# Performance work log

Hardware: AMD Instinct MI355X
Metric: run time of the kernel (lower is better)

Reference implementation:

```python
import jax, jax.numpy as jnp
import numpy as np

LOG2PI = float(np.log(2.0 * np.pi))
EPS_SHIFT = -0.5   # self.eps
TAU = 0.5          # self.tau
ETA = 1.0          # self.eta
MAG_A = 5500.0     # magnitude remap constants from forward()
MAG_B = 1100.0


def setup_inputs() -> dict:
    key = jax.random.key(0)
    k1, k2, k3, k4, k5 = jax.random.split(key, 5)
    B, K, C = 4096, 128, 64
    z = jax.random.normal(k1, (B, K, 2), dtype=jnp.float32)
    # per-keypoint mixture weights summing to 1 (GMM weights_)
    weights = jax.nn.softmax(jax.random.normal(k2, (K, C), dtype=jnp.float32), axis=-1)
    means = jax.random.normal(k3, (K, C, 2), dtype=jnp.float32)
    # SPD covariances: A A^T + 0.2 I
    A = jax.random.normal(k4, (K, C, 2, 2), dtype=jnp.float32) * 0.3
    covs = jnp.einsum('kcij,kclj->kcil', A, A) + 0.2 * jnp.eye(2, dtype=jnp.float32)
    # latent_stats unnormalization factor per latent coordinate (2/(max-min))
    scale = jax.random.uniform(k5, (K, 2), dtype=jnp.float32, minval=0.5, maxval=2.0)
    return {"z": z, "weights": weights, "means": means, "covs": covs, "scale": scale}


def _gmm_pdf_and_grad(z, weights, means, covs):
    # z: [B,K,2]  weights: [K,C]  means: [K,C,2]  covs: [K,C,2,2]
    a = covs[..., 0, 0]; b = covs[..., 0, 1]
    c = covs[..., 1, 0]; d = covs[..., 1, 1]
    det = a * d - b * c                                  # [K,C]
    inv00 = d / det; inv01 = -b / det
    inv10 = -c / det; inv11 = a / det
    diff = z[:, :, None, :] - means[None]                # [B,K,C,2]
    d0 = diff[..., 0]; d1 = diff[..., 1]
    s0 = inv00 * d0 + inv01 * d1                         # Sigma^{-1} diff, [B,K,C]
    s1 = inv10 * d0 + inv11 * d1
    maha = d0 * s0 + d1 * s1                             # [B,K,C]
    logp = -0.5 * (maha + jnp.log(det) + 2.0 * LOG2PI)   # MVN log_prob (D=2)
    comp = weights[None] * jnp.exp(logp)                 # weighted component densities
    pdf = comp.sum(-1)                                   # [B,K]
    # analytic grad of pdf wrt z: sum_c comp_c * (-Sigma_c^{-1} (z-mu_c))
    g0 = -(comp * s0).sum(-1)
    g1 = -(comp * s1).sum(-1)
    grad = jnp.stack([g0, g1], axis=-1)                  # [B,K,2]
    return pdf, grad


def reference(z, weights, means, covs, scale):
    B, K, _ = z.shape
    pdf, grad = _gmm_pdf_and_grad(z, weights, means, covs)
    # densities duplicated per coordinate: [pdf_i, pdf_i] per keypoint -> [B, 2K]
    densities = jnp.repeat(pdf, 2, axis=-1)
    density_norm = jax.nn.sigmoid((densities + EPS_SHIFT) / TAU)
    # unnormalize_gradient: elementwise rescale into raw latent space
    grad_raw = grad * scale[None]                        # [B,K,2]
    nrm = jnp.linalg.norm(grad_raw, axis=-1, keepdims=True)  # [B,K,1]
    mag = jnp.exp((-nrm + MAG_A) / MAG_B)
    negexp_grad = (grad_raw / nrm) * mag                 # [B,K,2]
    return density_norm, ETA * negexp_grad.reshape(B, 2 * K)
```

## Files before the change

kernel.cpp:

```cpp
#include <hip/hip_runtime.h>

#define K_KP   128
#define C_COMP 64
#define KPB    4

typedef float v2f __attribute__((ext_vector_type(2)));

#if __has_builtin(__builtin_amdgcn_exp2f)
#define EXP2F(x) __builtin_amdgcn_exp2f(x)
#else
#define EXP2F(x) exp2f(x)
#endif
#if __has_builtin(__builtin_amdgcn_logf)
#define LOG2F_(x) __builtin_amdgcn_logf(x)
#else
#define LOG2F_(x) __log2f(x)
#endif
#if __has_builtin(__builtin_amdgcn_rcpf)
#define RCPF(x) __builtin_amdgcn_rcpf(x)
#else
#define RCPF(x) (1.0f/(x))
#endif
#if __has_builtin(__builtin_amdgcn_rsqf)
#define RSQF(x) __builtin_amdgcn_rsqf(x)
#else
#define RSQF(x) rsqrtf(x)
#endif

__device__ __forceinline__ float rlane(float v, int l) {
    union { float f; int i; } u; u.f = v;
    u.i = __builtin_amdgcn_readlane(u.i, l);
    return u.f;
}

#define EVAL(m0, m1, i00, i01, i11, lc)                                 \
    {                                                                   \
        v2f d0 = ZX - (m0);                                             \
        v2f d1 = ZY - (m1);                                             \
        v2f s0 = (i00) * d0 + (i01) * d1;   \
        v2f s1 = (i01) * d0 + (i11) * d1;                               \
        v2f arg = (lc) - d0 * s0 - d1 * s1;           \
        v2f e;                                                          \
        e.x = EXP2F(arg.x);                                             \
        e.y = EXP2F(arg.y);                                             \
        pdf += e;                                                       \
        G0  += e * s0;                                                  \
        G1  += e * s1;                                                  \
    }

__global__ __launch_bounds__(256, 4) void recovery_kernel(
    const float* __restrict__ z,
    const float* __restrict__ weights,
    const float* __restrict__ means,
    const float* __restrict__ covs,
    const float* __restrict__ scale,
    float* __restrict__ out, int B)
{
    const int t    = threadIdx.x;
    const int lane = t & 63;
    const int wv   = __builtin_amdgcn_readfirstlane(t >> 6);

    const int bid = blockIdx.x;
    const int swz = (bid & 7) * 128 + (bid >> 3);
    const int kb  = swz & 31;
    const int bb  = swz >> 5;
    const int k   = kb * KPB + wv;
    const int b0  = bb * 128;

    const float K2       = 0.72134752044f;
    const float LOG2_2PI = 2.6514961295f;
    const int g = k * C_COMP + lane;
    float  w  = weights[g];
    float2 m  = ((const float2*)means)[g];
    float4 cv = ((const float4*)covs)[g];
    float det  = cv.x * cv.w - cv.y * cv.z;
    float rdet = RCPF(det);
    float vm0  = m.x;
    float vm1  = m.y;
    float vi00 =  cv.w * rdet * K2;
    float vi01 = -cv.y * rdet * K2;
    float vi11 =  cv.x * rdet * K2;
    float vlc  = LOG2F_(w) - LOG2_2PI - 0.5f * LOG2F_(det);

    const float2* z2 = (const float2*)z;
    float2 za = z2[(size_t)(b0 + lane)      * K_KP + k];
    float2 zb = z2[(size_t)(b0 + lane + 64) * K_KP + k];
    v2f ZX = {za.x, zb.x};
    v2f ZY = {za.y, zb.y};
    v2f pdf = {0.f, 0.f}, G0 = {0.f, 0.f}, G1 = {0.f, 0.f};

#pragma unroll
    for (int c = 0; c < C_COMP; ++c) {
        float m0  = rlane(vm0, c);
        float m1  = rlane(vm1, c);
        float i00 = rlane(vi00, c);
        float i01 = rlane(vi01, c);
        float i11 = rlane(vi11, c);
        float lc  = rlane(vlc, c);
        EVAL(m0, m1, i00, i01, i11, lc);
    }

    float2 sc = ((const float2*)scale)[k];
    const float NEG_INV_K2 = -1.3862943611f;
    float f0 = sc.x * NEG_INV_K2;
    float f1 = sc.y * NEG_INV_K2;
    const int KK2 = 2 * K_KP;
    float* out0 = out;
    float* out1 = out + (size_t)B * KK2;

    float pdfj[2] = {pdf.x, pdf.y};
    float gs0j[2] = {G0.x, G0.y};
    float gs1j[2] = {G1.x, G1.y};
#pragma unroll
    for (int j = 0; j < 2; ++j) {
        int b = b0 + lane + j * 64;
        float x  = 2.0f * pdfj[j] - 1.0f;
        float ex = EXP2F(-1.44269504f * x);
        float dn = RCPF(1.0f + ex);
        float g0 = gs0j[j] * f0;
        float g1 = gs1j[j] * f1;
        float n2 = fmaf(g0, g0, g1 * g1);
        float rn = RSQF(n2);
        float nrm = n2 * rn;
        float mag = EXP2F(fmaf(nrm, -0.0013115409f, 7.2134752044f));
        float mm = rn * mag;
        ((float2*)(out0 + (size_t)b * KK2 + 2 * k))[0] = make_float2(dn, dn);
        ((float2*)(out1 + (size_t)b * KK2 + 2 * k))[0] = make_float2(g0 * mm, g1 * mm);
    }
}

extern "C" void kernel_launch(void* const* d_in, const int* in_sizes, int n_in,
                              void* d_out, int out_size, void* d_ws, size_t ws_size,
                              hipStream_t stream) {
    const float* z       = (const float*)d_in[0];
    const float* weights = (const float*)d_in[1];
    const float* means   = (const float*)d_in[2];
    const float* covs    = (const float*)d_in[3];
    const float* scale   = (const float*)d_in[4];
    float* out = (float*)d_out;

    int B = in_sizes[0] / (2 * K_KP);
    int grid = (K_KP / KPB) * (B / 128);
    recovery_kernel<<<grid, 256, 0, stream>>>(z, weights, means, covs, scale, out, B);
}
```

Baseline: 77.28 us.

## Precompute GMM component params in prep kernel and load via scalar records

Adds a prep kernel that computes the per-component inverse covariance, mean and log-constant once and packs them into interleaved 12-float records, two components per record, in the workspace. The main kernel then reads these wave-uniform records with vector loads that can go through scalar loads, instead of computing per-lane parameters and broadcasting them with six readlanes per component. This removes the readlane traffic and repeated per-block parameter math, at the cost of an extra kernel launch and a dependency on workspace size. The old readlane path is kept as a fallback when no workspace is available.

```diff
diff --git a/kernel.cpp b/kernel.cpp
--- a/kernel.cpp
+++ b/kernel.cpp
@@ -2,6 +2,8 @@
 
 #define K_KP   128
 #define C_COMP 64
+#define NPAIR  (C_COMP / 2)
+#define RECF   12
 #define KPB    4
 
 typedef float v2f __attribute__((ext_vector_type(2)));
@@ -48,7 +50,98 @@
         G1  += e * s1;                                                  \
     }
 
+#define EPILOGUE()                                                            \
+    {                                                                         \
+        float2 sc = ((const float2*)scale)[k];                                \
+        const float NEG_INV_K2 = -1.3862943611f;         \
+        float f0 = sc.x * NEG_INV_K2;                                         \
+        float f1 = sc.y * NEG_INV_K2;                                         \
+        const int KK2 = 2 * K_KP;                                             \
+        float* out0 = out;                                                    \
+        float* out1 = out + (size_t)B * KK2;                                  \
+        float pdfj[2] = {pdf.x, pdf.y};                                       \
+        float gs0j[2] = {G0.x, G0.y};                                         \
+        float gs1j[2] = {G1.x, G1.y};                                         \
+        _Pragma("unroll")                                                     \
+        for (int j = 0; j < 2; ++j) {                                         \
+            int b = b0 + lane + j * 64;                                       \
+            float x  = 2.0f * pdfj[j] - 1.0f;     \
+            float ex = EXP2F(-1.44269504f * x);                               \
+            float dn = RCPF(1.0f + ex);                                       \
+            float g0 = gs0j[j] * f0;                                          \
+            float g1 = gs1j[j] * f1;                                          \
+            float n2 = fmaf(g0, g0, g1 * g1);                                 \
+            float rn = RSQF(n2);                                              \
+            float nrm = n2 * rn;                                              \
+            float mag = EXP2F(fmaf(nrm, -0.0013115409f, 7.2134752044f));      \
+            float mm = rn * mag;                                              \
+            ((float2*)(out0 + (size_t)b * KK2 + 2 * k))[0] =                  \
+                make_float2(dn, dn);                                          \
+            ((float2*)(out1 + (size_t)b * KK2 + 2 * k))[0] =                  \
+                make_float2(g0 * mm, g1 * mm);                                \
+        }                                                                     \
+    }
+
+__global__ __launch_bounds__(256) void prep_kernel(
+    const float* __restrict__ weights,
+    const float* __restrict__ means,
+    const float* __restrict__ covs,
+    float* __restrict__ params)
+{
+    const float K2       = 0.72134752044f;
+    const float LOG2_2PI = 2.6514961295f;
+    int g = blockIdx.x * 256 + threadIdx.x;
+    int k = g >> 6, c = g & 63;
+    float  w  = weights[g];
+    float2 m  = ((const float2*)means)[g];
+    float4 cv = ((const float4*)covs)[g];
+    float det  = cv.x * cv.w - cv.y * cv.z;
+    float rdet = RCPF(det);
+    float i00 =  cv.w * rdet * K2;
+    float i01 = -cv.y * rdet * K2;
+    float i11 =  cv.x * rdet * K2;
+    float lc  = LOG2F_(w) - LOG2_2PI - 0.5f * LOG2F_(det);
+    float* rec = params + ((size_t)k * NPAIR + (c >> 1)) * RECF;
+    ((float4*)rec)[c & 1] = make_float4(m.x, m.y, i00, i01);
+    ((float2*)(rec + 8))[c & 1] = make_float2(i11, lc);
+}
+
 __global__ __launch_bounds__(256, 4) void recovery_kernel(
+    const float* __restrict__ z,
+    const float* __restrict__ params,
+    const float* __restrict__ scale,
+    float* __restrict__ out, int B)
+{
+    const int t    = threadIdx.x;
+    const int lane = t & 63;
+    const int wv   = __builtin_amdgcn_readfirstlane(t >> 6);
+    const int bid = blockIdx.x;
+    const int swz = (bid & 7) * 128 + (bid >> 3);
+    const int kb  = swz & 31;
+    const int bb  = swz >> 5;
+    const int k   = kb * KPB + wv;
+    const int b0  = bb * 128;
+
+    const float2* z2 = (const float2*)z;
+    float2 za = z2[(size_t)(b0 + lane)      * K_KP + k];
+    float2 zb = z2[(size_t)(b0 + lane + 64) * K_KP + k];
+    v2f ZX = {za.x, zb.x};
+    v2f ZY = {za.y, zb.y};
+    v2f pdf = {0.f, 0.f}, G0 = {0.f, 0.f}, G1 = {0.f, 0.f};
+
+    const float* __restrict__ kp = params + (size_t)k * (NPAIR * RECF);
+#pragma unroll
+    for (int p = 0; p < NPAIR; ++p) {
+        float4 A0 = *(const float4*)(kp + p * RECF);
+        float4 A1 = *(const float4*)(kp + p * RECF + 4);
+        float4 Bp = *(const float4*)(kp + p * RECF + 8);
+        EVAL(A0.x, A0.y, A0.z, A0.w, Bp.x, Bp.y);
+        EVAL(A1.x, A1.y, A1.z, A1.w, Bp.z, Bp.w);
+    }
+    EPILOGUE();
+}
+
+__global__ __launch_bounds__(256, 4) void recovery_kernel_rl(
     const float* __restrict__ z,
     const float* __restrict__ weights,
     const float* __restrict__ means,
@@ -59,7 +152,6 @@
     const int t    = threadIdx.x;
     const int lane = t & 63;
     const int wv   = __builtin_amdgcn_readfirstlane(t >> 6);
-
     const int bid = blockIdx.x;
     const int swz = (bid & 7) * 128 + (bid >> 3);
     const int kb  = swz & 31;
@@ -99,34 +191,7 @@
         float lc  = rlane(vlc, c);
         EVAL(m0, m1, i00, i01, i11, lc);
     }
-
-    float2 sc = ((const float2*)scale)[k];
-    const float NEG_INV_K2 = -1.3862943611f;
-    float f0 = sc.x * NEG_INV_K2;
-    float f1 = sc.y * NEG_INV_K2;
-    const int KK2 = 2 * K_KP;
-    float* out0 = out;
-    float* out1 = out + (size_t)B * KK2;
-
-    float pdfj[2] = {pdf.x, pdf.y};
-    float gs0j[2] = {G0.x, G0.y};
-    float gs1j[2] = {G1.x, G1.y};
-#pragma unroll
-    for (int j = 0; j < 2; ++j) {
-        int b = b0 + lane + j * 64;
-        float x  = 2.0f * pdfj[j] - 1.0f;
-        float ex = EXP2F(-1.44269504f * x);
-        float dn = RCPF(1.0f + ex);
-        float g0 = gs0j[j] * f0;
-        float g1 = gs1j[j] * f1;
-        float n2 = fmaf(g0, g0, g1 * g1);
-        float rn = RSQF(n2);
-        float nrm = n2 * rn;
-        float mag = EXP2F(fmaf(nrm, -0.0013115409f, 7.2134752044f));
-        float mm = rn * mag;
-        ((float2*)(out0 + (size_t)b * KK2 + 2 * k))[0] = make_float2(dn, dn);
-        ((float2*)(out1 + (size_t)b * KK2 + 2 * k))[0] = make_float2(g0 * mm, g1 * mm);
-    }
+    EPILOGUE();
 }
 
 extern "C" void kernel_launch(void* const* d_in, const int* in_sizes, int n_in,
@@ -141,5 +206,13 @@
 
     int B = in_sizes[0] / (2 * K_KP);
     int grid = (K_KP / KPB) * (B / 128);
-    recovery_kernel<<<grid, 256, 0, stream>>>(z, weights, means, covs, scale, out, B);
-}
+
+    const size_t PARAM_BYTES = (size_t)K_KP * NPAIR * RECF * sizeof(float);
+    if (d_ws && ws_size >= PARAM_BYTES) {
+        float* params = (float*)d_ws;
+        prep_kernel<<<(K_KP * C_COMP) / 256, 256, 0, stream>>>(weights, means, covs, params);
+        recovery_kernel<<<grid, 256, 0, stream>>>(z, params, scale, out, B);
+    } else {
+        recovery_kernel_rl<<<grid, 256, 0, stream>>>(z, weights, means, covs, scale, out, B);
+    }
+}
```

Result: no change. 77.80 us (+0.7%).
